# Kernel optimization log

Measured on AMD Instinct MI355X. Metric: run time of the kernel, lower is better.

## Reference

```python
import jax, jax.numpy as jnp
import numpy as np

EPS = 1e-5


def tbn(x, g, b):
    # TensorBatchNorm2d(121): normalize each of the 11x11 tensor entries over (B, C, H, W)
    mu = x.mean(axis=(0, 1, 2, 3), keepdims=True)
    var = ((x - mu) ** 2).mean(axis=(0, 1, 2, 3), keepdims=True)
    return (x - mu) * jax.lax.rsqrt(var + EPS) * g + b


def prelu(x, a):
    return jnp.where(x >= 0, x, a * x)


def tconv1x1(x, U, V):
    # x: [B,1,H,W,m,n]; U: [p,m]; V: [q,n] -> y[...,p,q] = U @ X @ V^T
    return jnp.einsum('bchwmn,pm,qn->bchwpq', x, U, V)


def tconv3x3(x, U, V):
    # x: [B,1,H,W,m,n]; U,V: [3,3,p,m] / [3,3,q,n]; pad=1, stride=1
    H, W = x.shape[2], x.shape[3]
    xp = jnp.pad(x, ((0, 0), (0, 0), (1, 1), (1, 1), (0, 0), (0, 0)))
    y = jnp.zeros(x.shape[:4] + (U.shape[2], V.shape[2]), x.dtype)
    for i in range(3):
        for j in range(3):
            y = y + jnp.einsum('bchwmn,pm,qn->bchwpq', xp[:, :, i:i + H, j:j + W], U[i, j], V[i, j])
    return y


def forward(x, f0_U, f0_V, f0_g, f0_b, f0_a, s_U, s_V, s_g, s_b,
            blk_U1, blk_V1, blk_g1, blk_b1, blk_a1,
            blk_U2, blk_V2, blk_g2, blk_b2, blk_a2,
            blk_U3, blk_V3, blk_g3, blk_b3, head_W):
    # view(-1,8,16,16,32,32).permute(0,1,4,5,2,3) -> [B,8,32,32,16,16]
    x = x.reshape(-1, 8, 16, 16, 32, 32).transpose(0, 1, 4, 5, 2, 3)
    B, H, W = x.shape[0], 32, 32
    # f0: 3x3 tensorized conv, 8 channels -> 1, tensor 16x16 -> 11x11
    xp = jnp.pad(x, ((0, 0), (0, 0), (1, 1), (1, 1), (0, 0), (0, 0)))
    y = jnp.zeros((B, H, W, 11, 11), x.dtype)
    for i in range(3):
        for j in range(3):
            y = y + jnp.einsum('bchwmn,cpm,cqn->bhwpq', xp[:, :, i:i + H, j:j + W], f0_U[:, i, j], f0_V[:, i, j])
    h = prelu(tbn(y[:, None], f0_g, f0_b), f0_a)  # [B,1,32,32,11,11]
    for k in range(4):  # four residual bottleneck blocks with 1x1 shortcut
        idn = tbn(tconv1x1(h, s_U[k], s_V[k]), s_g[k], s_b[k])
        z = prelu(tbn(tconv1x1(h, blk_U1[k], blk_V1[k]), blk_g1[k], blk_b1[k]), blk_a1[k])
        z = prelu(tbn(tconv3x3(z, blk_U2[k], blk_V2[k]), blk_g2[k], blk_b2[k]), blk_a2[k])
        z = tbn(tconv1x1(z, blk_U3[k], blk_V3[k]), blk_g3[k], blk_b3[k])
        h = z + idn
    # fcn_head: 1x1, out_type=0 -> fully contract the [11,11] tensor per class
    return jnp.einsum('bchwmn,omn->bohw', h, head_W)  # [B,21,32,32]


def setup_inputs():
    ks = jax.random.split(jax.random.key(0), 26)
    r = lambda i, s: jax.random.normal(ks[i], s, dtype=jnp.float32)
    return {
        'x': r(0, (64, 8, 16, 16, 32, 32)),
        'f0_U': r(1, (8, 3, 3, 11, 16)) * 0.1,
        'f0_V': r(2, (8, 3, 3, 11, 16)) * 0.1,
        'f0_g': r(3, (11, 11)), 'f0_b': r(4, (11, 11)),
        'f0_a': jnp.float32(0.25),
        's_U': r(5, (4, 11, 11)) * 0.3, 's_V': r(6, (4, 11, 11)) * 0.3,
        's_g': r(7, (4, 11, 11)), 's_b': r(8, (4, 11, 11)),
        'blk_U1': r(9, (4, 11, 11)) * 0.3, 'blk_V1': r(10, (4, 11, 11)) * 0.3,
        'blk_g1': r(11, (4, 11, 11)), 'blk_b1': r(12, (4, 11, 11)),
        'blk_a1': jax.random.uniform(ks[13], (4,), dtype=jnp.float32),
        'blk_U2': r(14, (4, 3, 3, 11, 11)) * 0.2, 'blk_V2': r(15, (4, 3, 3, 11, 11)) * 0.2,
        'blk_g2': r(16, (4, 11, 11)), 'blk_b2': r(17, (4, 11, 11)),
        'blk_a2': jax.random.uniform(ks[18], (4,), dtype=jnp.float32),
        'blk_U3': r(19, (4, 11, 11)) * 0.3, 'blk_V3': r(20, (4, 11, 11)) * 0.3,
        'blk_g3': r(21, (4, 11, 11)), 'blk_b3': r(22, (4, 11, 11)),
        'head_W': r(23, (21, 11, 11)) * 0.1,
    }


def reference(x, f0_U, f0_V, f0_g, f0_b, f0_a, s_U, s_V, s_g, s_b,
              blk_U1, blk_V1, blk_g1, blk_b1, blk_a1,
              blk_U2, blk_V2, blk_g2, blk_b2, blk_a2,
              blk_U3, blk_V3, blk_g3, blk_b3, head_W):
    return forward(x, f0_U, f0_V, f0_g, f0_b, f0_a, s_U, s_V, s_g, s_b,
                   blk_U1, blk_V1, blk_g1, blk_b1, blk_a1,
                   blk_U2, blk_V2, blk_g2, blk_b2, blk_a2,
                   blk_U3, blk_V3, blk_g3, blk_b3, head_W)
```

## Files before the change

### kernel.cpp

```cpp
#include <hip/hip_runtime.h>

#define NPOS 65536
#define NE   121
#define NP   6

__device__ __forceinline__ void gload_lds16(const float* g, float* l) {
  __builtin_amdgcn_global_load_lds(
      (const __attribute__((address_space(1))) void*)g,
      (__attribute__((address_space(3))) void*)l, 16, 0, 0);
}

__global__ __launch_bounds__(256, 1)
void f0_kernel(const float* __restrict__ x, const float* __restrict__ U,
               const float* __restrict__ V, float* __restrict__ y) {
  __shared__ float Xb[16384];
  __shared__ float su[1152];
  __shared__ float sv[1728];

  int bid = blockIdx.x;
  int wg  = (bid & 7) * 512 + (bid >> 3);
  int ph  = wg & 1;
  int row = wg >> 1;
  int b = row >> 5, h = row & 31;
  int P0 = ph * 5;
  int t = threadIdx.x;
  int s = t >> 5, w = t & 31;

  int hlo = (h == 0) ? 0 : h - 1;
  int hhi = (h == 31) ? 31 : h + 1;
  int nh = hhi - hlo + 1;
  int nslab = 8 * nh;

  float Y[NP][11];
#pragma unroll
  for (int p = 0; p < NP; ++p)
#pragma unroll
    for (int q = 0; q < 11; ++q) Y[p][q] = 0.f;

  auto stageUV = [&](int c) {
    for (int idx = t; idx < 1152; idx += 256) {
      int tap = idx >> 7, r = idx & 127;
      int m = r >> 3, pr = r & 7;
      su[idx] = (pr < 6) ? U[(c * 9 + tap) * 176 + (P0 + pr) * 16 + m] : 0.f;
    }
    for (int idx = t; idx < 1728; idx += 256) {
      int tap = idx / 192, r = idx - tap * 192;
      int n = r / 12, q = r - n * 12;
      sv[idx] = (q < 11) ? V[(c * 9 + tap) * 176 + q * 16 + n] : 0.f;
    }
  };

  auto issueX = [&](int k) {
    int c = k / nh, hi = hlo + k % nh;
    const float* base = x + ((size_t)(b * 8 + c) << 18) + hi * 32;
    float* buf = &Xb[(k & 1) * 8192];
    int wv = t >> 6, lane = t & 63;
#pragma unroll
    for (int kk = 0; kk < 8; ++kk) {
      int chunk = wv * 8 + kk;
      int mn = chunk * 8 + (lane >> 3);
      gload_lds16(base + (size_t)mn * 1024 + (lane & 7) * 4,
                  buf + chunk * 256);
    }
  };

  stageUV(0);
  issueX(0);

  for (int k = 0; k < nslab; ++k) {
    asm volatile("s_waitcnt vmcnt(0)" ::: "memory");
    __syncthreads();
    if (k + 1 < nslab) issueX(k + 1);

    const float* Xt = &Xb[(k & 1) * 8192];
    int c = k / nh, hi = hlo + k % nh;
    int tapbase = (hi - h + 1) * 3;
#pragma unroll
    for (int j = 0; j < 3; ++j) {
      int wj = w + j - 1;
      if ((unsigned)wj < 32u) {
        int tap = tapbase + j;
        const float* suT = &su[tap * 128];
        const float* svT = &sv[tap * 192];
        float A0[6], A1[6];
#pragma unroll
        for (int p = 0; p < 6; ++p) { A0[p] = 0.f; A1[p] = 0.f; }
#pragma unroll
        for (int m = 0; m < 16; ++m) {
          float x0 = Xt[(m * 16 + 2 * s) * 32 + wj];
          float x1 = Xt[(m * 16 + 2 * s + 1) * 32 + wj];
          float4 u0 = *(const float4*)&suT[m * 8];
          float2 u1 = *(const float2*)&suT[m * 8 + 4];
          A0[0] += u0.x * x0; A1[0] += u0.x * x1;
          A0[1] += u0.y * x0; A1[1] += u0.y * x1;
          A0[2] += u0.z * x0; A1[2] += u0.z * x1;
          A0[3] += u0.w * x0; A1[3] += u0.w * x1;
          A0[4] += u1.x * x0; A1[4] += u1.x * x1;
          A0[5] += u1.y * x0; A1[5] += u1.y * x1;
        }
#pragma unroll
        for (int nn = 0; nn < 2; ++nn) {
          const float* vb = &svT[(2 * s + nn) * 12];
          float4 v0 = *(const float4*)&vb[0];
          float4 v1 = *(const float4*)&vb[4];
          float4 v2 = *(const float4*)&vb[8];
          float vq[11] = { v0.x, v0.y, v0.z, v0.w,
                           v1.x, v1.y, v1.z, v1.w,
                           v2.x, v2.y, v2.z };
          const float* Ax = nn ? A1 : A0;
#pragma unroll
          for (int p = 0; p < 6; ++p)
#pragma unroll
            for (int q = 0; q < 11; ++q)
              Y[p][q] += Ax[p] * vq[q];
        }
      }
    }
    if (k + 1 < nslab && (k % nh) == nh - 1) {
      __syncthreads();
      stageUV(c + 1);
    }
  }

  int posb = ((b << 5) + h) << 5;
#pragma unroll
  for (int p = 0; p < NP; ++p) {
    __syncthreads();
#pragma unroll
    for (int q = 0; q < 11; ++q) Xb[t * 11 + q] = Y[p][q];
    __syncthreads();
    for (int idx = t; idx < 352; idx += 256) {
      int qq = idx >> 5, w2 = idx & 31;
      float ssum = 0.f;
#pragma unroll
      for (int s2 = 0; s2 < 8; ++s2) ssum += Xb[(s2 * 32 + w2) * 11 + qq];
      y[(size_t)((P0 + p) * 11 + qq) * NPOS + posb + w2] = ssum;
    }
  }
}

__global__ __launch_bounds__(256)
void stats_kernel(const float* __restrict__ raw, const float* __restrict__ g,
                  const float* __restrict__ bb, float* __restrict__ sc,
                  float* __restrict__ sh) {
  int e = blockIdx.x;
  const float4* p = (const float4*)(raw + (size_t)e * NPOS);
  int t = threadIdx.x;
  float s = 0.f, s2 = 0.f;
  for (int i = t; i < 16384; i += 256) {
    float4 v = p[i];
    s  += v.x + v.y + v.z + v.w;
    s2 += v.x * v.x + v.y * v.y + v.z * v.z + v.w * v.w;
  }
#pragma unroll
  for (int o = 32; o > 0; o >>= 1) {
    s  += __shfl_down(s, o);
    s2 += __shfl_down(s2, o);
  }
  __shared__ float ls[8];
  int wid = t >> 6;
  if ((t & 63) == 0) { ls[wid] = s; ls[4 + wid] = s2; }
  __syncthreads();
  if (t == 0) {
    float ss  = ls[0] + ls[1] + ls[2] + ls[3];
    float ss2 = ls[4] + ls[5] + ls[6] + ls[7];
    float mu  = ss  * (1.f / 65536.f);
    float var = ss2 * (1.f / 65536.f) - mu * mu;
    float sca = g[e] * rsqrtf(var + 1e-5f);
    sc[e] = sca;
    sh[e] = bb[e] - mu * sca;
  }
}

template<bool HASB, bool PRELU>
__global__ __launch_bounds__(256, 2)
void conv1x1_kernel(const float* __restrict__ rA, const float* __restrict__ scA,
                    const float* __restrict__ shA,
                    const float* __restrict__ rB, const float* __restrict__ scB,
                    const float* __restrict__ shB,
                    const float* __restrict__ alpha_ptr, int alpha_idx,
                    const float* __restrict__ U, const float* __restrict__ V,
                    float* __restrict__ out) {
  __shared__ float su[NP * 11], sv[121], sa[242], sb[242];
  int bid = blockIdx.x;
  int wg  = (bid & 7) * 64 + (bid >> 3);
  int ph = wg & 1, posblk = wg >> 1;
  int P0 = ph * 5;
  int t = threadIdx.x;
  if (t < 121) {
    sv[t] = V[t];
    sa[t] = scA[t]; sb[t] = shA[t];
    if (HASB) { sa[121 + t] = scB[t]; sb[121 + t] = shB[t]; }
  }
  if (t < NP * 11) su[t] = U[P0 * 11 + t];
  __syncthreads();
  float alpha = 0.f;
  if (PRELU) alpha = alpha_ptr[alpha_idx];
  size_t pos = (size_t)posblk * 256 + t;

  float T[NP][11];
#pragma unroll
  for (int p = 0; p < NP; ++p)
#pragma unroll
    for (int n = 0; n < 11; ++n) T[p][n] = 0.f;

#pragma unroll 2
  for (int m = 0; m < 11; ++m) {
    float Xr[11];
#pragma unroll
    for (int n = 0; n < 11; ++n) {
      int e = m * 11 + n;
      float v = sa[e] * rA[(size_t)e * NPOS + pos] + sb[e];
      if (HASB) v += sa[121 + e] * rB[(size_t)e * NPOS + pos] + sb[121 + e];
      if (PRELU) v = v >= 0.f ? v : alpha * v;
      Xr[n] = v;
    }
#pragma unroll
    for (int p = 0; p < NP; ++p) {
      float u = su[p * 11 + m];
#pragma unroll
      for (int n = 0; n < 11; ++n) T[p][n] += u * Xr[n];
    }
  }
#pragma unroll
  for (int q = 0; q < 11; ++q) {
    float Yc[NP];
#pragma unroll
    for (int p = 0; p < NP; ++p) Yc[p] = 0.f;
#pragma unroll
    for (int n = 0; n < 11; ++n) {
      float v = sv[q * 11 + n];
#pragma unroll
      for (int p = 0; p < NP; ++p) Yc[p] += T[p][n] * v;
    }
#pragma unroll
    for (int p = 0; p < NP; ++p)
      out[(size_t)((P0 + p) * 11 + q) * NPOS + pos] = Yc[p];
  }
}

template<int N0, int NW>
__device__ __forceinline__ void c3_chunk(const float* __restrict__ rA,
    const float* __restrict__ sa, const float* __restrict__ sh,
    const float* __restrict__ su, const float* __restrict__ sv,
    float alpha, int npos, float (&Y)[NP][11]) {
  float T[NP][NW];
#pragma unroll
  for (int p = 0; p < NP; ++p)
#pragma unroll
    for (int k = 0; k < NW; ++k) T[p][k] = 0.f;
#pragma unroll 2
  for (int m = 0; m < 11; ++m) {
    float Xr[NW];
#pragma unroll
    for (int k = 0; k < NW; ++k) {
      int e = m * 11 + N0 + k;
      float v = sa[e] * rA[(size_t)e * NPOS + npos] + sh[e];
      Xr[k] = v >= 0.f ? v : alpha * v;
    }
#pragma unroll
    for (int p = 0; p < NP; ++p) {
      float u = su[p * 11 + m];
#pragma unroll
      for (int k = 0; k < NW; ++k) T[p][k] += u * Xr[k];
    }
  }
#pragma unroll
  for (int k = 0; k < NW; ++k) {
#pragma unroll
    for (int q = 0; q < 11; ++q) {
      float v = sv[q * 11 + N0 + k];
#pragma unroll
      for (int p = 0; p < NP; ++p) Y[p][q] += T[p][k] * v;
    }
  }
}

__global__ __launch_bounds__(256, 2)
void conv3x3_kernel(const float* __restrict__ rA, const float* __restrict__ scA,
                    const float* __restrict__ shA,
                    const float* __restrict__ alpha_ptr, int alpha_idx,
                    const float* __restrict__ U, const float* __restrict__ V,
                    float* __restrict__ out) {
  __shared__ float su[9 * NP * 11], sv[1089], sa[121], sh[121];
  int bid = blockIdx.x;
  int wg  = (bid & 7) * 64 + (bid >> 3);
  int ph = wg & 1, posblk = wg >> 1;
  int P0 = ph * 5;
  int t = threadIdx.x;
  for (int idx = t; idx < 9 * NP * 11; idx += 256) {
    int ij = idx / (NP * 11), r = idx - ij * (NP * 11);
    su[idx] = U[ij * 121 + P0 * 11 + r];
  }
  for (int idx = t; idx < 1089; idx += 256) sv[idx] = V[idx];
  if (t < 121) { sa[t] = scA[t]; sh[t] = shA[t]; }
  __syncthreads();
  float alpha = alpha_ptr[alpha_idx];
  int pos = posblk * 256 + t;
  int b = pos >> 10, h = (pos >> 5) & 31, w = pos & 31;

  float Y[NP][11];
#pragma unroll
  for (int p = 0; p < NP; ++p)
#pragma unroll
    for (int q = 0; q < 11; ++q) Y[p][q] = 0.f;

  for (int ij = 0; ij < 9; ++ij) {
    int i = ij / 3, j = ij - 3 * (ij / 3);
    int hi = h + i - 1, wj = w + j - 1;
    if ((unsigned)hi >= 32u || (unsigned)wj >= 32u) continue;
    int npos = ((b << 5) + hi) * 32 + wj;
    const float* suij = &su[ij * NP * 11];
    const float* svij = &sv[ij * 121];
    c3_chunk<0, 4>(rA, sa, sh, suij, svij, alpha, npos, Y);
    c3_chunk<4, 4>(rA, sa, sh, suij, svij, alpha, npos, Y);
    c3_chunk<8, 3>(rA, sa, sh, suij, svij, alpha, npos, Y);
  }
#pragma unroll
  for (int p = 0; p < NP; ++p)
#pragma unroll
    for (int q = 0; q < 11; ++q)
      out[(size_t)((P0 + p) * 11 + q) * NPOS + pos] = Y[p][q];
}

__global__ __launch_bounds__(256, 2)
void head_kernel(const float* __restrict__ rA, const float* __restrict__ scA,
                 const float* __restrict__ shA,
                 const float* __restrict__ rB, const float* __restrict__ scB,
                 const float* __restrict__ shB,
                 const float* __restrict__ W, float* __restrict__ out) {
  __shared__ float sw[21 * 121], sa[242], sh[242];
  int t = threadIdx.x;
  for (int idx = t; idx < 2541; idx += 256) sw[idx] = W[idx];
  if (t < 121) {
    sa[t] = scA[t]; sh[t] = shA[t];
    sa[121 + t] = scB[t]; sh[121 + t] = shB[t];
  }
  __syncthreads();
  size_t pos = (size_t)blockIdx.x * 256 + t;
  int b = (int)(pos >> 10), hw = (int)(pos & 1023);
  float acc[21];
#pragma unroll
  for (int o = 0; o < 21; ++o) acc[o] = 0.f;
  for (int e = 0; e < 121; ++e) {
    float v = sa[e] * rA[(size_t)e * NPOS + pos] + sh[e] +
              sa[121 + e] * rB[(size_t)e * NPOS + pos] + sh[121 + e];
#pragma unroll
    for (int o = 0; o < 21; ++o) acc[o] += v * sw[o * 121 + e];
  }
#pragma unroll
  for (int o = 0; o < 21; ++o)
    out[(size_t)(b * 21 + o) * 1024 + hw] = acc[o];
}

extern "C" void kernel_launch(void* const* d_in, const int* in_sizes, int n_in,
                              void* d_out, int out_size, void* d_ws, size_t ws_size,
                              hipStream_t stream) {
  (void)in_sizes; (void)n_in; (void)out_size; (void)ws_size;
  const float* x     = (const float*)d_in[0];
  const float* f0_U  = (const float*)d_in[1];
  const float* f0_V  = (const float*)d_in[2];
  const float* f0_g  = (const float*)d_in[3];
  const float* f0_b  = (const float*)d_in[4];
  const float* f0_a  = (const float*)d_in[5];
  const float* s_U   = (const float*)d_in[6];
  const float* s_V   = (const float*)d_in[7];
  const float* s_g   = (const float*)d_in[8];
  const float* s_b   = (const float*)d_in[9];
  const float* bU1   = (const float*)d_in[10];
  const float* bV1   = (const float*)d_in[11];
  const float* bg1   = (const float*)d_in[12];
  const float* bb1   = (const float*)d_in[13];
  const float* ba1   = (const float*)d_in[14];
  const float* bU2   = (const float*)d_in[15];
  const float* bV2   = (const float*)d_in[16];
  const float* bg2   = (const float*)d_in[17];
  const float* bb2   = (const float*)d_in[18];
  const float* ba2   = (const float*)d_in[19];
  const float* bU3   = (const float*)d_in[20];
  const float* bV3   = (const float*)d_in[21];
  const float* bg3   = (const float*)d_in[22];
  const float* bb3   = (const float*)d_in[23];
  const float* headW = (const float*)d_in[24];

  float* ws = (float*)d_ws;
  const size_t BUF = (size_t)NE * NPOS;
  float* B[4] = { ws, ws + BUF, ws + 2 * BUF, ws + 3 * BUF };
  float* st   = ws + 4 * BUF;

  auto SCp = [&](int op) { return st + op * 242; };
  auto SHp = [&](int op) { return st + op * 242 + 121; };
  auto run_stats = [&](const float* raw, const float* g, const float* bb, int op) {
    stats_kernel<<<121, 256, 0, stream>>>(raw, g, bb, SCp(op), SHp(op));
  };

  f0_kernel<<<4096, 256, 0, stream>>>(x, f0_U, f0_V, B[0]);
  run_stats(B[0], f0_g, f0_b, 0);

  const int bufs[4][4] = { {1,2,3,0}, {2,3,0,1}, {3,0,1,2}, {0,1,2,3} };

  const float* hA   = B[0];  const float* hAsc = SCp(0); const float* hAsh = SHp(0);
  const float* hB   = nullptr; const float* hBsc = nullptr; const float* hBsh = nullptr;

  for (int k = 0; k < 4; ++k) {
    float* idn = B[bufs[k][0]];
    float* z1  = B[bufs[k][1]];
    float* z2  = B[bufs[k][2]];
    float* z3  = B[bufs[k][3]];
    int op_idn = 1 + k * 4, op_z1 = 2 + k * 4, op_z2 = 3 + k * 4, op_z3 = 4 + k * 4;

    if (k == 0) {
      conv1x1_kernel<false, true><<<512, 256, 0, stream>>>(
          hA, hAsc, hAsh, nullptr, nullptr, nullptr, f0_a, 0,
          s_U + k * 121, s_V + k * 121, idn);
      conv1x1_kernel<false, true><<<512, 256, 0, stream>>>(
          hA, hAsc, hAsh, nullptr, nullptr, nullptr, f0_a, 0,
          bU1 + k * 121, bV1 + k * 121, z1);
    } else {
      conv1x1_kernel<true, false><<<512, 256, 0, stream>>>(
          hA, hAsc, hAsh, hB, hBsc, hBsh, nullptr, 0,
          s_U + k * 121, s_V + k * 121, idn);
      conv1x1_kernel<true, false><<<512, 256, 0, stream>>>(
          hA, hAsc, hAsh, hB, hBsc, hBsh, nullptr, 0,
          bU1 + k * 121, bV1 + k * 121, z1);
    }
    run_stats(idn, s_g + k * 121, s_b + k * 121, op_idn);
    run_stats(z1,  bg1 + k * 121, bb1 + k * 121, op_z1);

    conv3x3_kernel<<<512, 256, 0, stream>>>(
        z1, SCp(op_z1), SHp(op_z1), ba1, k,
        bU2 + k * 1089, bV2 + k * 1089, z2);
    run_stats(z2, bg2 + k * 121, bb2 + k * 121, op_z2);

    conv1x1_kernel<false, true><<<512, 256, 0, stream>>>(
        z2, SCp(op_z2), SHp(op_z2), nullptr, nullptr, nullptr, ba2, k,
        bU3 + k * 121, bV3 + k * 121, z3);
    run_stats(z3, bg3 + k * 121, bb3 + k * 121, op_z3);

    hA = z3;  hAsc = SCp(op_z3);  hAsh = SHp(op_z3);
    hB = idn; hBsc = SCp(op_idn); hBsh = SHp(op_idn);
  }

  head_kernel<<<256, 256, 0, stream>>>(hA, hAsc, hAsh, hB, hBsc, hBsh,
                                       headW, (float*)d_out);
}
```

Baseline: 1.873 ms.

## Share X loads across taps via lane shuffles and fuse f0 BN partial stats

The f0 conv loop now reads each X value once per slab, at the thread's own column. It computes U-contractions for all three horizontal taps and moves the left and right tap results to neighbouring lanes with cross-lane shuffles, zeroing them at the edges. This replaces three separate shifted LDS reads per tap. U is now read directly from global memory instead of being staged in shared memory. The epilogue also produces per-row partial sums and sums of squares, which a small finalize kernel reduces, replacing the full-pass stats kernel over the f0 output. The trade-offs are more registers and uncached-pattern global reads of U, and the E[x²]-mu² variance formula is less numerically stable.

```diff
diff --git a/kernel.cpp b/kernel.cpp
--- a/kernel.cpp
+++ b/kernel.cpp
@@ -12,9 +12,9 @@
 
 __global__ __launch_bounds__(256, 1)
 void f0_kernel(const float* __restrict__ x, const float* __restrict__ U,
-               const float* __restrict__ V, float* __restrict__ y) {
+               const float* __restrict__ V, float* __restrict__ y,
+               float* __restrict__ psum, float* __restrict__ psq) {
   __shared__ float Xb[16384];
-  __shared__ float su[1152];
   __shared__ float sv[1728];
 
   int bid = blockIdx.x;
@@ -25,6 +25,7 @@
   int P0 = ph * 5;
   int t = threadIdx.x;
   int s = t >> 5, w = t & 31;
+  int lane = t & 63;
 
   int hlo = (h == 0) ? 0 : h - 1;
   int hhi = (h == 31) ? 31 : h + 1;
@@ -37,12 +38,7 @@
 #pragma unroll
     for (int q = 0; q < 11; ++q) Y[p][q] = 0.f;
 
-  auto stageUV = [&](int c) {
-    for (int idx = t; idx < 1152; idx += 256) {
-      int tap = idx >> 7, r = idx & 127;
-      int m = r >> 3, pr = r & 7;
-      su[idx] = (pr < 6) ? U[(c * 9 + tap) * 176 + (P0 + pr) * 16 + m] : 0.f;
-    }
+  auto stageV = [&](int c) {
     for (int idx = t; idx < 1728; idx += 256) {
       int tap = idx / 192, r = idx - tap * 192;
       int n = r / 12, q = r - n * 12;
@@ -54,17 +50,16 @@
     int c = k / nh, hi = hlo + k % nh;
     const float* base = x + ((size_t)(b * 8 + c) << 18) + hi * 32;
     float* buf = &Xb[(k & 1) * 8192];
-    int wv = t >> 6, lane = t & 63;
+    int wv = t >> 6, ln = t & 63;
 #pragma unroll
     for (int kk = 0; kk < 8; ++kk) {
       int chunk = wv * 8 + kk;
-      int mn = chunk * 8 + (lane >> 3);
-      gload_lds16(base + (size_t)mn * 1024 + (lane & 7) * 4,
-                  buf + chunk * 256);
+      int mn = chunk * 8 + (ln >> 3);
+      gload_lds16(base + (size_t)mn * 1024 + (ln & 7) * 4, buf + chunk * 256);
     }
   };
 
-  stageUV(0);
+  stageV(0);
   issueX(0);
 
   for (int k = 0; k < nslab; ++k) {
@@ -75,50 +70,61 @@
     const float* Xt = &Xb[(k & 1) * 8192];
     int c = k / nh, hi = hlo + k % nh;
     int tapbase = (hi - h + 1) * 3;
+    const float* Ug = U + ((c * 9 + tapbase) * 176 + P0 * 16);
+
+    float A[3][6][2];
+#pragma unroll
+    for (int j = 0; j < 3; ++j)
+#pragma unroll
+      for (int p = 0; p < 6; ++p) { A[j][p][0] = 0.f; A[j][p][1] = 0.f; }
+
+#pragma unroll
+    for (int m = 0; m < 16; ++m) {
+      float x0 = Xt[(m * 16 + 2 * s) * 32 + w];
+      float x1 = Xt[(m * 16 + 2 * s + 1) * 32 + w];
+#pragma unroll
+      for (int j = 0; j < 3; ++j)
+#pragma unroll
+        for (int p = 0; p < 6; ++p) {
+          float u = Ug[j * 176 + p * 16 + m];
+          A[j][p][0] += u * x0;
+          A[j][p][1] += u * x1;
+        }
+    }
+#pragma unroll
+    for (int p = 0; p < 6; ++p)
+#pragma unroll
+      for (int nn = 0; nn < 2; ++nn) {
+        float a0 = __shfl(A[0][p][nn], lane - 1, 64);
+        float a2 = __shfl(A[2][p][nn], lane + 1, 64);
+        A[0][p][nn] = (w == 0)  ? 0.f : a0;
+        A[2][p][nn] = (w == 31) ? 0.f : a2;
+      }
 #pragma unroll
     for (int j = 0; j < 3; ++j) {
-      int wj = w + j - 1;
-      if ((unsigned)wj < 32u) {
-        int tap = tapbase + j;
-        const float* suT = &su[tap * 128];
-        const float* svT = &sv[tap * 192];
-        float A0[6], A1[6];
-#pragma unroll
-        for (int p = 0; p < 6; ++p) { A0[p] = 0.f; A1[p] = 0.f; }
-#pragma unroll
-        for (int m = 0; m < 16; ++m) {
-          float x0 = Xt[(m * 16 + 2 * s) * 32 + wj];
-          float x1 = Xt[(m * 16 + 2 * s + 1) * 32 + wj];
-          float4 u0 = *(const float4*)&suT[m * 8];
-          float2 u1 = *(const float2*)&suT[m * 8 + 4];
-          A0[0] += u0.x * x0; A1[0] += u0.x * x1;
-          A0[1] += u0.y * x0; A1[1] += u0.y * x1;
-          A0[2] += u0.z * x0; A1[2] += u0.z * x1;
-          A0[3] += u0.w * x0; A1[3] += u0.w * x1;
-          A0[4] += u1.x * x0; A1[4] += u1.x * x1;
-          A0[5] += u1.y * x0; A1[5] += u1.y * x1;
-        }
-#pragma unroll
-        for (int nn = 0; nn < 2; ++nn) {
-          const float* vb = &svT[(2 * s + nn) * 12];
-          float4 v0 = *(const float4*)&vb[0];
-          float4 v1 = *(const float4*)&vb[4];
-          float4 v2 = *(const float4*)&vb[8];
-          float vq[11] = { v0.x, v0.y, v0.z, v0.w,
-                           v1.x, v1.y, v1.z, v1.w,
-                           v2.x, v2.y, v2.z };
-          const float* Ax = nn ? A1 : A0;
-#pragma unroll
-          for (int p = 0; p < 6; ++p)
-#pragma unroll
-            for (int q = 0; q < 11; ++q)
-              Y[p][q] += Ax[p] * vq[q];
+      int tap = tapbase + j;
+#pragma unroll
+      for (int nn = 0; nn < 2; ++nn) {
+        const float* vb = &sv[tap * 192 + (2 * s + nn) * 12];
+        float4 v0 = *(const float4*)&vb[0];
+        float4 v1 = *(const float4*)&vb[4];
+        float4 v2 = *(const float4*)&vb[8];
+        float vq[11] = { v0.x, v0.y, v0.z, v0.w,
+                         v1.x, v1.y, v1.z, v1.w,
+                         v2.x, v2.y, v2.z };
+#pragma unroll
+        for (int p = 0; p < 6; ++p) {
+          float a = A[j][p][nn];
+#pragma unroll
+          for (int q = 0; q < 11; ++q)
+            Y[p][q] += a * vq[q];
         }
       }
     }
+
     if (k + 1 < nslab && (k % nh) == nh - 1) {
       __syncthreads();
-      stageUV(c + 1);
+      stageV(c + 1);
     }
   }
 
@@ -129,13 +135,57 @@
 #pragma unroll
     for (int q = 0; q < 11; ++q) Xb[t * 11 + q] = Y[p][q];
     __syncthreads();
-    for (int idx = t; idx < 352; idx += 256) {
-      int qq = idx >> 5, w2 = idx & 31;
-      float ssum = 0.f;
-#pragma unroll
-      for (int s2 = 0; s2 < 8; ++s2) ssum += Xb[(s2 * 32 + w2) * 11 + qq];
-      y[(size_t)((P0 + p) * 11 + qq) * NPOS + posb + w2] = ssum;
-    }
+    for (int rep = 0; rep < 2; ++rep) {
+      int idx = rep * 256 + t;
+      if (idx < 352) {
+        int qq = idx >> 5, w2 = idx & 31;
+        float v = 0.f;
+#pragma unroll
+        for (int s2 = 0; s2 < 8; ++s2) v += Xb[(s2 * 32 + w2) * 11 + qq];
+        int e = (P0 + p) * 11 + qq;
+        y[(size_t)e * NPOS + posb + w2] = v;
+        float sm = v, sq = v * v;
+#pragma unroll
+        for (int d = 16; d > 0; d >>= 1) {
+          sm += __shfl_down(sm, d, 32);
+          sq += __shfl_down(sq, d, 32);
+        }
+        if (w2 == 0) {
+          psum[(size_t)e * 2048 + row] = sm;
+          psq [(size_t)e * 2048 + row] = sq;
+        }
+      }
+    }
+  }
+}
+
+__global__ __launch_bounds__(256)
+void f0_stats_final(const float* __restrict__ psum, const float* __restrict__ psq,
+                    const float* __restrict__ g, const float* __restrict__ bb,
+                    float* __restrict__ sc, float* __restrict__ sh) {
+  int e = blockIdx.x, t = threadIdx.x;
+  float s = 0.f, s2 = 0.f;
+  for (int i = t; i < 2048; i += 256) {
+    s  += psum[(size_t)e * 2048 + i];
+    s2 += psq [(size_t)e * 2048 + i];
+  }
+#pragma unroll
+  for (int o = 32; o > 0; o >>= 1) {
+    s  += __shfl_down(s, o);
+    s2 += __shfl_down(s2, o);
+  }
+  __shared__ float ls[8];
+  int wid = t >> 6;
+  if ((t & 63) == 0) { ls[wid] = s; ls[4 + wid] = s2; }
+  __syncthreads();
+  if (t == 0) {
+    float ss  = ls[0] + ls[1] + ls[2] + ls[3];
+    float ss2 = ls[4] + ls[5] + ls[6] + ls[7];
+    float mu  = ss  * (1.f / 65536.f);
+    float var = ss2 * (1.f / 65536.f) - mu * mu;
+    float sca = g[e] * rsqrtf(var + 1e-5f);
+    sc[e] = sca;
+    sh[e] = bb[e] - mu * sca;
   }
 }
 
@@ -385,8 +435,10 @@
 
   float* ws = (float*)d_ws;
   const size_t BUF = (size_t)NE * NPOS;
-  float* B[4] = { ws, ws + BUF, ws + 2 * BUF, ws + 3 * BUF };
-  float* st   = ws + 4 * BUF;
+  float* B[4]  = { ws, ws + BUF, ws + 2 * BUF, ws + 3 * BUF };
+  float* st    = ws + 4 * BUF;
+  float* psum  = st + 17 * 242;
+  float* psq   = psum + 121 * 2048;
 
   auto SCp = [&](int op) { return st + op * 242; };
   auto SHp = [&](int op) { return st + op * 242 + 121; };
@@ -394,8 +446,8 @@
     stats_kernel<<<121, 256, 0, stream>>>(raw, g, bb, SCp(op), SHp(op));
   };
 
-  f0_kernel<<<4096, 256, 0, stream>>>(x, f0_U, f0_V, B[0]);
-  run_stats(B[0], f0_g, f0_b, 0);
+  f0_kernel<<<4096, 256, 0, stream>>>(x, f0_U, f0_V, B[0], psum, psq);
+  f0_stats_final<<<121, 256, 0, stream>>>(psum, psq, f0_g, f0_b, SCp(0), SHp(0));
 
   const int bufs[4][4] = { {1,2,3,0}, {2,3,0,1}, {3,0,1,2}, {0,1,2,3} };
 
```

Measured after the change: 4.176 ms. 2.23x slower.
